# Kernel optimization log

Hardware: AMD Instinct MI355X
Metric: run time of the kernel (lower is better)

Reference implementation:

```python
import jax, jax.numpy as jnp
import numpy as np

SIZE_DICT = 1024
DIM_DICT = 256
BETA = 0.001


def setup_inputs() -> dict:
    key = jax.random.key(0)
    k1, k2 = jax.random.split(key)
    z = jax.random.normal(k1, (64, 1024, DIM_DICT), dtype=jnp.float32)
    codebook = jax.random.normal(k2, (SIZE_DICT, DIM_DICT), dtype=jnp.float32)
    return {"z": z, "codebook": codebook, "flg_train": 1}


def reference(z, codebook, flg_train):
    zf = z.reshape(-1, DIM_DICT)  # [N, D]
    # squared euclidean distances: ||z||^2 + ||c||^2 - 2 z c^T  -> [N, K]
    d = (jnp.sum(zf ** 2, axis=1, keepdims=True)
         + jnp.sum(codebook ** 2, axis=1)
         - 2.0 * jnp.matmul(zf, codebook.T))
    idx = jnp.argmin(d, axis=1)  # [N]
    # one-hot @ codebook == gather
    z_q = codebook[idx].reshape(z.shape)
    if flg_train:
        loss = (jnp.mean((jax.lax.stop_gradient(z_q) - z) ** 2)
                + BETA * jnp.mean((z_q - jax.lax.stop_gradient(z)) ** 2))
    else:
        loss = jnp.float32(0.0)
    # straight-through estimator
    z_q = z + jax.lax.stop_gradient(z_q - z)
    # perplexity from codebook usage histogram (== mean of one-hot rows)
    n = zf.shape[0]
    counts = jax.ops.segment_sum(jnp.ones((n,), jnp.float32), idx,
                                 num_segments=SIZE_DICT)
    e_mean = counts / n
    perplexity = jnp.exp(-jnp.sum(e_mean * jnp.log(e_mean + 1e-10)))
    return (z_q, loss, perplexity)
```

## Files before the change

kernel.cpp:

```cpp
#include <hip/hip_runtime.h>


#define N_ROWS 65536
#define DIM    256
#define K_CODES 1024
#define BETA   0.001f

#define BM      128
#define NBLOCKS (N_ROWS / BM)
#define NTHREADS 512
#define CHUNK_BYTES 65536
#define NCHUNK  16

#define LO_SCALE 2048.0f
#define LO_INV   (1.0f / 2048.0f)

#define WS_BESTS_OFF 16384
#define WS_CBIMG_OFF 278528
#define WS_NEED (WS_CBIMG_OFF + NCHUNK * CHUNK_BYTES)

typedef _Float16 f16x8 __attribute__((ext_vector_type(8)));
typedef float f32x16 __attribute__((ext_vector_type(16)));


__global__ void cnorm_kernel(const float* __restrict__ cb, float* __restrict__ cnorm) {
    int k = blockIdx.x * blockDim.x + threadIdx.x;
    if (k >= K_CODES) return;
    const float4* row = (const float4*)(cb + (size_t)k * DIM);
    float s = 0.f;
#pragma unroll
    for (int j = 0; j < DIM / 4; ++j) {
        float4 v = row[j];
        s = fmaf(v.x, v.x, s);
        s = fmaf(v.y, v.y, s);
        s = fmaf(v.z, v.z, s);
        s = fmaf(v.w, v.w, s);
    }
    cnorm[k] = s;
}

__global__ void cb_prep(const float* __restrict__ cb, char* __restrict__ img) {
    int idx = blockIdx.x * blockDim.x + threadIdx.x;
    int c   = idx >> 5;
    int g32 = idx & 31;
    const float4* src = (const float4*)(cb + (size_t)c * DIM + g32 * 8);
    float4 v0 = src[0], v1 = src[1];
    float vv[8] = {v0.x, v0.y, v0.z, v0.w, v1.x, v1.y, v1.z, v1.w};
    f16x8 hi, lo;
#pragma unroll
    for (int j = 0; j < 8; ++j) {
        _Float16 h = (_Float16)vv[j];
        hi[j] = h;
        lo[j] = (_Float16)((vv[j] - (float)h) * LO_SCALE);
    }
    int kh = g32 >> 4;
    int gl = g32 & 15;
    int cl = c & 63;
    int unit = (c >> 6) * 2 + kh;
    size_t off = (size_t)unit * 32768 + (size_t)gl * 1024 + (size_t)cl * 16;
    *(f16x8*)(img + off) = hi;
    *(f16x8*)(img + off + 16384) = lo;
}


__device__ inline void stage_chunk(const char* img, int c, char* ldsbase, int tid) {
#pragma unroll
    for (int i = 0; i < 8; ++i) {
        __builtin_amdgcn_global_load_lds(
            (const __attribute__((address_space(1))) unsigned int*)
                (img + (size_t)c * CHUNK_BYTES + i * 8192 + tid * 16),
            (__attribute__((address_space(3))) unsigned int*)
                (ldsbase + i * 8192 + tid * 16),
            16, 0, 0);
    }
}

#define LOADB(KS, BH, BL)                                                            \
    {                                                                                \
        const _Float16* p = bbase + ((KS) >> 3) * 16384 + (((KS) & 7) * 2 + lh) * 512;\
        BH = *(const f16x8*)(p);                                                     \
        BL = *(const f16x8*)(p + 8192);                                              \
    }

#define MF3(KS, BH, BL)                                                              \
    {                                                                                \
        f16x8 ah = zh[KS], al = zl[KS];                                              \
        acc_hh = __builtin_amdgcn_mfma_f32_32x32x16_f16(ah, BH, acc_hh, 0, 0, 0);    \
        acc_x1 = __builtin_amdgcn_mfma_f32_32x32x16_f16(ah, BL, acc_x1, 0, 0, 0);    \
        acc_x2 = __builtin_amdgcn_mfma_f32_32x32x16_f16(al, BH, acc_x2, 0, 0, 0);    \
    }

#define PHASE(P)                                                                     \
    {                                                                                \
        f16x8 bh0, bl0, bh1, bl1, bh2, bl2, bh3, bl3;                                \
        LOADB((P) * 4 + 0, bh0, bl0)                                                 \
        LOADB((P) * 4 + 1, bh1, bl1)                                                 \
        LOADB((P) * 4 + 2, bh2, bl2)                                                 \
        LOADB((P) * 4 + 3, bh3, bl3)                                                 \
        if ((P) == 0 && c + 1 < NCHUNK)                                              \
            stage_chunk(img, c + 1, (char*)csb + (b ^ 1) * CHUNK_BYTES, tid);        \
        asm volatile("" ::: "memory");                                               \
        __builtin_amdgcn_s_barrier();                                                \
        asm volatile("" ::: "memory");                                               \
        __builtin_amdgcn_s_setprio(1);                                               \
        MF3((P) * 4 + 0, bh0, bl0)                                                   \
        MF3((P) * 4 + 1, bh1, bl1)                                                   \
        MF3((P) * 4 + 2, bh2, bl2)                                                   \
        MF3((P) * 4 + 3, bh3, bl3)                                                   \
        __builtin_amdgcn_s_setprio(0);                                               \
        if ((P) == 3)                                                                \
            asm volatile("s_waitcnt vmcnt(0)" ::: "memory");                         \
        asm volatile("" ::: "memory");                                               \
        __builtin_amdgcn_s_barrier();                                                \
        asm volatile("" ::: "memory");                                               \
    }

__global__ __launch_bounds__(NTHREADS, 2)
void vq_main_mfma(const float* __restrict__ z, const char* __restrict__ img,
                  const float* __restrict__ cnorm, int* __restrict__ bests_g,
                  int* __restrict__ counts, float* __restrict__ ploss) {
    __shared__ _Float16 csb[2 * 32768];
    __shared__ float bs2[BM][2];
    __shared__ int   bc2[BM][2];
    __shared__ float znorm_lds[BM];
    __shared__ float red[NTHREADS];

    const int tid  = threadIdx.x;
    const int lane = tid & 63;
    const int w    = tid >> 6;
    const int wr   = w >> 1;
    const int wc   = w & 1;
    const int l31  = lane & 31;
    const int lh   = lane >> 5;
    const int r0   = blockIdx.x * BM;

    stage_chunk(img, 0, (char*)csb, tid);

    const int zrow = wr * 32 + l31;
    f16x8 zh[16], zl[16];
    {
        const float* zr = z + (size_t)(r0 + zrow) * DIM;
        float zn = 0.f;
#pragma unroll
        for (int gi = 0; gi < 16; ++gi) {
            int g = gi * 2 + lh;
            float4 v0 = *(const float4*)(zr + g * 8);
            float4 v1 = *(const float4*)(zr + g * 8 + 4);
            float vv[8] = {v0.x, v0.y, v0.z, v0.w, v1.x, v1.y, v1.z, v1.w};
            f16x8 hi, lo;
#pragma unroll
            for (int j = 0; j < 8; ++j) {
                _Float16 h = (_Float16)vv[j];
                hi[j] = h;
                lo[j] = (_Float16)((vv[j] - (float)h) * LO_SCALE);
                zn = fmaf(vv[j], vv[j], zn);
            }
            zh[gi] = hi;
            zl[gi] = lo;
        }
        zn += __shfl_xor(zn, 32, 64);
        if (wc == 0 && lh == 0) znorm_lds[zrow] = zn;
    }

    asm volatile("s_waitcnt vmcnt(0)" ::: "memory");
    __builtin_amdgcn_s_barrier();
    asm volatile("" ::: "memory");

    f32x16 acc_hh, acc_x1, acc_x2;
#pragma unroll
    for (int e = 0; e < 16; ++e) { acc_hh[e] = 0.f; acc_x1[e] = 0.f; acc_x2[e] = 0.f; }
    float best_s[16];
    int   best_c[16];
#pragma unroll
    for (int e = 0; e < 16; ++e) { best_s[e] = 3.4e38f; best_c[e] = 0; }

    const int crow = wc * 32 + l31;

#pragma unroll 1
    for (int c = 0; c < NCHUNK; ++c) {
        const int b = c & 1;
        const _Float16* bbase = csb + b * 32768 + crow * 8;
        float cn = cnorm[c * 64 + crow];

        PHASE(0)
        PHASE(1)
        PHASE(2)
        PHASE(3)

        {
            int col = c * 64 + crow;
#pragma unroll
            for (int rg = 0; rg < 16; ++rg) {
                float dot = fmaf(acc_x1[rg] + acc_x2[rg], LO_INV, acc_hh[rg]);
                float s = fmaf(-2.0f, dot, cn);
                bool take = s < best_s[rg];
                best_s[rg] = take ? s : best_s[rg];
                best_c[rg] = take ? col : best_c[rg];
            }
#pragma unroll
            for (int e = 0; e < 16; ++e) { acc_hh[e] = 0.f; acc_x1[e] = 0.f; acc_x2[e] = 0.f; }
        }
    }

#pragma unroll
    for (int rg = 0; rg < 16; ++rg) {
        float bsv = best_s[rg];
        int   bcv = best_c[rg];
#pragma unroll
        for (int s = 1; s < 32; s <<= 1) {
            float os = __shfl_xor(bsv, s, 64);
            int   oc = __shfl_xor(bcv, s, 64);
            bool take = (os < bsv) || (os == bsv && oc < bcv);
            bsv = take ? os : bsv;
            bcv = take ? oc : bcv;
        }
        best_s[rg] = bsv;
        best_c[rg] = bcv;
    }
    if (l31 == 0) {
#pragma unroll
        for (int rg = 0; rg < 16; ++rg) {
            int rl = (rg & 3) + 8 * (rg >> 2) + 4 * lh;
            bs2[wr * 32 + rl][wc] = best_s[rg];
            bc2[wr * 32 + rl][wc] = best_c[rg];
        }
    }
    __syncthreads();

    float lsum = 0.f;
    if (tid < BM) {
        float s0 = bs2[tid][0], s1 = bs2[tid][1];
        int   c0 = bc2[tid][0], c1 = bc2[tid][1];
        bool t1 = (s1 < s0) || (s1 == s0 && c1 < c0);
        int   bc = t1 ? c1 : c0;
        float bs = t1 ? s1 : s0;
        bests_g[r0 + tid] = bc;
        atomicAdd(&counts[bc], 1);
        lsum = bs + znorm_lds[tid];
    }
    red[tid] = lsum;
    __syncthreads();
    for (int s = NTHREADS / 2; s > 0; s >>= 1) {
        if (tid < s) red[tid] += red[tid + s];
        __syncthreads();
    }
    if (tid == 0) ploss[blockIdx.x] = red[0];
}


__global__ __launch_bounds__(256)
void vq_gather(const float4* __restrict__ cb4, const int* __restrict__ bests,
               float4* __restrict__ out4) {
    int gid = blockIdx.x * blockDim.x + threadIdx.x;
    int row = gid >> 6;
    int q   = gid & 63;
    out4[gid] = cb4[(size_t)bests[row] * 64 + q];
}


#define FBM     32
#define FCHUNK  512
#define FDSTAGE 16
#define FCS_PAD 20
#define FNBLOCKS (N_ROWS / FBM)

__global__ __launch_bounds__(256, 2)
void vq_main_fp32(const float* __restrict__ z, const float* __restrict__ cb,
                  const float* __restrict__ cnorm, float* __restrict__ out,
                  int* __restrict__ counts, float* __restrict__ ploss) {
    __shared__ float zs[FBM][DIM];
    __shared__ float cs[FCHUNK][FCS_PAD];
    __shared__ int   bests[FBM];
    __shared__ float red[256];

    const int tid = threadIdx.x;
    const int tx  = tid & 63;
    const int ty  = tid >> 6;
    const int r0  = blockIdx.x * FBM;

    {
        const float4* zg  = (const float4*)(z + (size_t)r0 * DIM);
        float4*       zsv = (float4*)&zs[0][0];
#pragma unroll
        for (int j = 0; j < (FBM * DIM / 4) / 256; ++j)
            zsv[tid + 256 * j] = zg[tid + 256 * j];
    }

    unsigned long long best[8];
#pragma unroll
    for (int i = 0; i < 8; ++i) best[i] = ~0ull;

    for (int cb0 = 0; cb0 < K_CODES; cb0 += FCHUNK) {
        float acc[8][8];
#pragma unroll
        for (int i = 0; i < 8; ++i)
#pragma unroll
            for (int m = 0; m < 8; ++m) acc[i][m] = 0.f;

        for (int sd = 0; sd < DIM / FDSTAGE; ++sd) {
            __syncthreads();
#pragma unroll
            for (int j = 0; j < 8; ++j) {
                int f4i = tid + 256 * j;
                int c   = f4i >> 2;
                int qq  = f4i & 3;
                float4 v = *(const float4*)(cb + (size_t)(cb0 + c) * DIM + sd * FDSTAGE + qq * 4);
                *(float4*)&cs[c][qq * 4] = v;
            }
            __syncthreads();

#pragma unroll
            for (int dd4 = 0; dd4 < FDSTAGE / 4; ++dd4) {
                float4 zv[8], cv[8];
#pragma unroll
                for (int i = 0; i < 8; ++i)
                    zv[i] = *(const float4*)&zs[ty * 8 + i][sd * FDSTAGE + dd4 * 4];
#pragma unroll
                for (int m = 0; m < 8; ++m)
                    cv[m] = *(const float4*)&cs[tx + 64 * m][dd4 * 4];
#pragma unroll
                for (int i = 0; i < 8; ++i)
#pragma unroll
                    for (int m = 0; m < 8; ++m) {
                        float a = acc[i][m];
                        a = fmaf(zv[i].x, cv[m].x, a);
                        a = fmaf(zv[i].y, cv[m].y, a);
                        a = fmaf(zv[i].z, cv[m].z, a);
                        a = fmaf(zv[i].w, cv[m].w, a);
                        acc[i][m] = a;
                    }
            }
        }

#pragma unroll
        for (int m = 0; m < 8; ++m) {
            int   c  = cb0 + tx + 64 * m;
            float cn = cnorm[c];
#pragma unroll
            for (int i = 0; i < 8; ++i) {
                float s = fmaf(-2.f, acc[i][m], cn);
                unsigned u = __float_as_uint(s);
                u = (u & 0x80000000u) ? ~u : (u | 0x80000000u);
                unsigned long long key = ((unsigned long long)u << 32) | (unsigned)c;
                best[i] = key < best[i] ? key : best[i];
            }
        }
    }

#pragma unroll
    for (int i = 0; i < 8; ++i) {
        unsigned long long b = best[i];
#pragma unroll
        for (int s = 1; s < 64; s <<= 1) {
            unsigned long long o = __shfl_xor(b, s, 64);
            b = o < b ? o : b;
        }
        best[i] = b;
    }
    if (tx == 0)
#pragma unroll
        for (int i = 0; i < 8; ++i)
            bests[ty * 8 + i] = (int)(best[i] & 0xFFFFFFFFu);
    __syncthreads();

    const int r  = tid >> 3;
    const int lq = tid & 7;
    const int bidx = bests[r];
    const float4* crow = (const float4*)(cb + (size_t)bidx * DIM);
    const float4* zrow = (const float4*)&zs[r][0];
    float4*       orow = (float4*)(out + (size_t)(r0 + r) * DIM);
    float lsum = 0.f;
#pragma unroll
    for (int j = 0; j < 8; ++j) {
        int qg = lq + j * 8;
        float4 c4 = crow[qg];
        float4 z4 = zrow[qg];
        float4 o;
        float dx = c4.x - z4.x; o.x = z4.x + dx; lsum = fmaf(dx, dx, lsum);
        float dy = c4.y - z4.y; o.y = z4.y + dy; lsum = fmaf(dy, dy, lsum);
        float dz = c4.z - z4.z; o.z = z4.z + dz; lsum = fmaf(dz, dz, lsum);
        float dw = c4.w - z4.w; o.w = z4.w + dw; lsum = fmaf(dw, dw, lsum);
        orow[qg] = o;
    }
    if (tid < FBM) atomicAdd(&counts[bests[tid]], 1);

    red[tid] = lsum;
    __syncthreads();
    for (int s = 128; s > 0; s >>= 1) {
        if (tid < s) red[tid] += red[tid + s];
        __syncthreads();
    }
    if (tid == 0) ploss[blockIdx.x] = red[0];
}


__global__ void vq_final(const float* __restrict__ ploss, const int* __restrict__ counts,
                         const int* __restrict__ flg, float* __restrict__ out2, int np) {
    __shared__ float red[1024];
    const int t = threadIdx.x;

    float l = 0.f;
    for (int i = t; i < np; i += 1024) l += ploss[i];
    red[t] = l;
    __syncthreads();
    for (int s = 512; s > 0; s >>= 1) {
        if (t < s) red[t] += red[t + s];
        __syncthreads();
    }
    if (t == 0) {
        float loss = (red[0] / (float)((size_t)N_ROWS * DIM)) * (1.0f + BETA);
        if (flg[0] == 0) loss = 0.f;
        out2[0] = loss;
    }
    __syncthreads();

    float e = (float)counts[t] / (float)N_ROWS;
    red[t] = e * logf(e + 1e-10f);
    __syncthreads();
    for (int s = 512; s > 0; s >>= 1) {
        if (t < s) red[t] += red[t + s];
        __syncthreads();
    }
    if (t == 0) out2[1] = expf(-red[0]);
}

extern "C" void kernel_launch(void* const* d_in, const int* in_sizes, int n_in,
                              void* d_out, int out_size, void* d_ws, size_t ws_size,
                              hipStream_t stream) {
    const float* z   = (const float*)d_in[0];
    const float* cb  = (const float*)d_in[1];
    const int*   flg = (const int*)d_in[2];
    float* out = (float*)d_out;
    float* ws  = (float*)d_ws;

    float* cnorm  = ws;
    int*   counts = (int*)((char*)d_ws + 4096);
    float* ploss  = (float*)((char*)d_ws + 8192);
    int*   bests  = (int*)((char*)d_ws + WS_BESTS_OFF);
    char*  cbimg  = (char*)d_ws + WS_CBIMG_OFF;

    hipMemsetAsync(counts, 0, K_CODES * sizeof(int), stream);
    cnorm_kernel<<<K_CODES / 256, 256, 0, stream>>>(cb, cnorm);

    if (ws_size >= (size_t)WS_NEED) {
        cb_prep<<<128, 256, 0, stream>>>(cb, cbimg);
        vq_main_mfma<<<NBLOCKS, NTHREADS, 0, stream>>>(z, cbimg, cnorm, bests, counts, ploss);
        vq_gather<<<(N_ROWS * 64) / 256, 256, 0, stream>>>((const float4*)cb, bests, (float4*)out);
        vq_final<<<1, 1024, 0, stream>>>(ploss, counts, flg, out + (size_t)N_ROWS * DIM, NBLOCKS);
    } else {
        vq_main_fp32<<<FNBLOCKS, 256, 0, stream>>>(z, cb, cnorm, out, counts, ploss);
        vq_final<<<1, 1024, 0, stream>>>(ploss, counts, flg, out + (size_t)N_ROWS * DIM, FNBLOCKS);
    }
}
```

Before: 176.8 us.

## Stage codebook per-wave into private LDS slots to eliminate block barriers

Replaces the block-wide double-buffered 64KB chunk staging with per-wave private LDS buffers: each wave loads only the codebook slices it consumes, in quarter-chunk units, double-buffered and synchronized with vmcnt waits instead of s_barrier. It also caches the codebook norms in LDS up front. The goal is to remove the two workgroup barriers per phase so waves run decoupled and overlap loads with MFMA. The cost is that both waves sharing a column half now load duplicate data, which raises global/L2 traffic, and the pipeline depth per wave is small.

```diff
diff --git a/kernel.cpp b/kernel.cpp
--- a/kernel.cpp
+++ b/kernel.cpp
@@ -9,15 +9,13 @@
 #define BM      128
 #define NBLOCKS (N_ROWS / BM)
 #define NTHREADS 512
-#define CHUNK_BYTES 65536
-#define NCHUNK  16
 
 #define LO_SCALE 2048.0f
 #define LO_INV   (1.0f / 2048.0f)
 
 #define WS_BESTS_OFF 16384
 #define WS_CBIMG_OFF 278528
-#define WS_NEED (WS_CBIMG_OFF + NCHUNK * CHUNK_BYTES)
+#define WS_NEED (WS_CBIMG_OFF + 32 * 32768)
 
 typedef _Float16 f16x8 __attribute__((ext_vector_type(8)));
 typedef float f32x16 __attribute__((ext_vector_type(16)));
@@ -56,30 +54,37 @@
     int kh = g32 >> 4;
     int gl = g32 & 15;
     int cl = c & 63;
-    int unit = (c >> 6) * 2 + kh;
-    size_t off = (size_t)unit * 32768 + (size_t)gl * 1024 + (size_t)cl * 16;
+    int iu = (c >> 6) * 2 + kh;
+    size_t off = (size_t)iu * 32768 + (size_t)gl * 1024 + (size_t)cl * 16;
     *(f16x8*)(img + off) = hi;
     *(f16x8*)(img + off + 16384) = lo;
 }
 
 
-__device__ inline void stage_chunk(const char* img, int c, char* ldsbase, int tid) {
-#pragma unroll
-    for (int i = 0; i < 8; ++i) {
+__device__ inline void stage_u(const char* __restrict__ img, int s, int wc,
+                               int lane, char* dst) {
+    int chunk = s >> 2, q = s & 3;
+    const char* base = img + (size_t)(chunk * 2 + (q >> 1)) * 32768
+                     + (size_t)((q & 1) * 8) * 1024 + wc * 512
+                     + (lane >> 5) * 1024 + (lane & 31) * 16;
+#pragma unroll
+    for (int i = 0; i < 4; ++i) {
         __builtin_amdgcn_global_load_lds(
-            (const __attribute__((address_space(1))) unsigned int*)
-                (img + (size_t)c * CHUNK_BYTES + i * 8192 + tid * 16),
-            (__attribute__((address_space(3))) unsigned int*)
-                (ldsbase + i * 8192 + tid * 16),
+            (const __attribute__((address_space(1))) unsigned int*)(base + i * 2048),
+            (__attribute__((address_space(3))) unsigned int*)(dst + i * 1024),
             16, 0, 0);
-    }
-}
-
-#define LOADB(KS, BH, BL)                                                            \
+        __builtin_amdgcn_global_load_lds(
+            (const __attribute__((address_space(1))) unsigned int*)(base + 16384 + i * 2048),
+            (__attribute__((address_space(3))) unsigned int*)(dst + 4096 + i * 1024),
+            16, 0, 0);
+    }
+}
+
+#define LOADB_U(R, BH, BL)                                                           \
     {                                                                                \
-        const _Float16* p = bbase + ((KS) >> 3) * 16384 + (((KS) & 7) * 2 + lh) * 512;\
+        const _Float16* p = ub + ((R) * 2 + lh) * 256 + l31 * 8;                     \
         BH = *(const f16x8*)(p);                                                     \
-        BL = *(const f16x8*)(p + 8192);                                              \
+        BL = *(const f16x8*)(p + 2048);                                              \
     }
 
 #define MF3(KS, BH, BL)                                                              \
@@ -90,36 +95,51 @@
         acc_x2 = __builtin_amdgcn_mfma_f32_32x32x16_f16(al, BH, acc_x2, 0, 0, 0);    \
     }
 
-#define PHASE(P)                                                                     \
+#define UNIT_PHASE(CHUNK, Q, WAITN, DOSTAGE)                                         \
     {                                                                                \
+        asm volatile("s_waitcnt vmcnt(" #WAITN ")" ::: "memory");                    \
+        const _Float16* ub = wlds + ((Q) & 1) * 4096;                                \
         f16x8 bh0, bl0, bh1, bl1, bh2, bl2, bh3, bl3;                                \
-        LOADB((P) * 4 + 0, bh0, bl0)                                                 \
-        LOADB((P) * 4 + 1, bh1, bl1)                                                 \
-        LOADB((P) * 4 + 2, bh2, bl2)                                                 \
-        LOADB((P) * 4 + 3, bh3, bl3)                                                 \
-        if ((P) == 0 && c + 1 < NCHUNK)                                              \
-            stage_chunk(img, c + 1, (char*)csb + (b ^ 1) * CHUNK_BYTES, tid);        \
-        asm volatile("" ::: "memory");                                               \
-        __builtin_amdgcn_s_barrier();                                                \
-        asm volatile("" ::: "memory");                                               \
+        LOADB_U(0, bh0, bl0)                                                         \
+        LOADB_U(1, bh1, bl1)                                                         \
+        LOADB_U(2, bh2, bl2)                                                         \
+        LOADB_U(3, bh3, bl3)                                                         \
+        asm volatile("s_waitcnt lgkmcnt(0)" ::: "memory");                           \
+        if (DOSTAGE)                                                                 \
+            stage_u(img, (CHUNK) * 4 + (Q) + 2, wc, lane,                            \
+                    (char*)wlds + ((Q) & 1) * 8192);                                 \
         __builtin_amdgcn_s_setprio(1);                                               \
-        MF3((P) * 4 + 0, bh0, bl0)                                                   \
-        MF3((P) * 4 + 1, bh1, bl1)                                                   \
-        MF3((P) * 4 + 2, bh2, bl2)                                                   \
-        MF3((P) * 4 + 3, bh3, bl3)                                                   \
+        MF3((Q) * 4 + 0, bh0, bl0)                                                   \
+        MF3((Q) * 4 + 1, bh1, bl1)                                                   \
+        MF3((Q) * 4 + 2, bh2, bl2)                                                   \
+        MF3((Q) * 4 + 3, bh3, bl3)                                                   \
         __builtin_amdgcn_s_setprio(0);                                               \
-        if ((P) == 3)                                                                \
-            asm volatile("s_waitcnt vmcnt(0)" ::: "memory");                         \
-        asm volatile("" ::: "memory");                                               \
-        __builtin_amdgcn_s_barrier();                                                \
-        asm volatile("" ::: "memory");                                               \
+    }
+
+#define FOLD(CHUNK)                                                                  \
+    {                                                                                \
+        int col = (CHUNK) * 64 + crow;                                               \
+        float cn = cnorm_lds[col];                                                   \
+        _Pragma("unroll")                                                            \
+        for (int rg = 0; rg < 16; ++rg) {                                            \
+            float dot = fmaf(acc_x1[rg] + acc_x2[rg], LO_INV, acc_hh[rg]);           \
+            float s = fmaf(-2.0f, dot, cn);                                          \
+            bool take = s < best_s[rg];                                              \
+            best_s[rg] = take ? s : best_s[rg];                                      \
+            best_c[rg] = take ? col : best_c[rg];                                    \
+        }                                                                            \
+        _Pragma("unroll")                                                            \
+        for (int e = 0; e < 16; ++e) {                                               \
+            acc_hh[e] = 0.f; acc_x1[e] = 0.f; acc_x2[e] = 0.f;                       \
+        }                                                                            \
     }
 
 __global__ __launch_bounds__(NTHREADS, 2)
 void vq_main_mfma(const float* __restrict__ z, const char* __restrict__ img,
                   const float* __restrict__ cnorm, int* __restrict__ bests_g,
                   int* __restrict__ counts, float* __restrict__ ploss) {
-    __shared__ _Float16 csb[2 * 32768];
+    __shared__ _Float16 csb[8 * 8192];
+    __shared__ float cnorm_lds[1024];
     __shared__ float bs2[BM][2];
     __shared__ int   bc2[BM][2];
     __shared__ float znorm_lds[BM];
@@ -134,7 +154,7 @@
     const int lh   = lane >> 5;
     const int r0   = blockIdx.x * BM;
 
-    stage_chunk(img, 0, (char*)csb, tid);
+    _Float16* wlds = csb + w * 8192;
 
     const int zrow = wr * 32 + l31;
     f16x8 zh[16], zl[16];
@@ -162,9 +182,12 @@
         if (wc == 0 && lh == 0) znorm_lds[zrow] = zn;
     }
 
-    asm volatile("s_waitcnt vmcnt(0)" ::: "memory");
-    __builtin_amdgcn_s_barrier();
-    asm volatile("" ::: "memory");
+    cnorm_lds[tid]       = cnorm[tid];
+    cnorm_lds[tid + 512] = cnorm[tid + 512];
+    __syncthreads();
+
+    stage_u(img, 0, wc, lane, (char*)wlds);
+    stage_u(img, 1, wc, lane, (char*)wlds + 8192);
 
     f32x16 acc_hh, acc_x1, acc_x2;
 #pragma unroll
@@ -177,30 +200,18 @@
     const int crow = wc * 32 + l31;
 
 #pragma unroll 1
-    for (int c = 0; c < NCHUNK; ++c) {
-        const int b = c & 1;
-        const _Float16* bbase = csb + b * 32768 + crow * 8;
-        float cn = cnorm[c * 64 + crow];
-
-        PHASE(0)
-        PHASE(1)
-        PHASE(2)
-        PHASE(3)
-
-        {
-            int col = c * 64 + crow;
-#pragma unroll
-            for (int rg = 0; rg < 16; ++rg) {
-                float dot = fmaf(acc_x1[rg] + acc_x2[rg], LO_INV, acc_hh[rg]);
-                float s = fmaf(-2.0f, dot, cn);
-                bool take = s < best_s[rg];
-                best_s[rg] = take ? s : best_s[rg];
-                best_c[rg] = take ? col : best_c[rg];
-            }
-#pragma unroll
-            for (int e = 0; e < 16; ++e) { acc_hh[e] = 0.f; acc_x1[e] = 0.f; acc_x2[e] = 0.f; }
-        }
-    }
+    for (int chunk = 0; chunk < 15; ++chunk) {
+        UNIT_PHASE(chunk, 0, 8, 1)
+        UNIT_PHASE(chunk, 1, 8, 1)
+        UNIT_PHASE(chunk, 2, 8, 1)
+        UNIT_PHASE(chunk, 3, 8, 1)
+        FOLD(chunk)
+    }
+    UNIT_PHASE(15, 0, 8, 1)
+    UNIT_PHASE(15, 1, 8, 1)
+    UNIT_PHASE(15, 2, 8, 0)
+    UNIT_PHASE(15, 3, 0, 0)
+    FOLD(15)
 
 #pragma unroll
     for (int rg = 0; rg < 16; ++rg) {
```

Measured after the change: 208.0 us. 1.18x slower.
